# Optimization experiments

Hardware: AMD Instinct MI355X
Metric: run time of the kernel (lower is better)

Reference implementation:

```python
import math
import jax, jax.numpy as jnp
import numpy as np

HIDDEN = 768
N_HEADS = 12
HEAD_DIM = HIDDEN // N_HEADS


def _alibi_slopes(num_heads: int) -> np.ndarray:
    def pow2_slopes(n):
        start = 2.0 ** (-2.0 ** (-(math.log2(n) - 3)))
        return start ** np.arange(1, n + 1, dtype=np.float32)
    if math.log2(num_heads).is_integer():
        return pow2_slopes(num_heads).astype(np.float32)
    closest = 2 ** math.floor(math.log2(num_heads))
    base = pow2_slopes(closest)
    extra = pow2_slopes(2 * closest)[0::2][: num_heads - closest]
    return np.concatenate([base, extra], axis=0).astype(np.float32)

ALIBI_SLOPES = jnp.asarray(_alibi_slopes(N_HEADS))


def setup_inputs() -> dict:
    key = jax.random.key(0)
    ks = jax.random.split(key, 7)
    B, S = 4, 2048
    scale = 1.0 / math.sqrt(HIDDEN)
    inp = {
        "hidden_states": jax.random.normal(ks[0], (B, S, HIDDEN), dtype=jnp.float32),
        "Wq": jax.random.normal(ks[1], (HIDDEN, HIDDEN), dtype=jnp.float32) * scale,
        "bq": jnp.zeros((HIDDEN,), dtype=jnp.float32),
        "Wk": jax.random.normal(ks[2], (HIDDEN, HIDDEN), dtype=jnp.float32) * scale,
        "bk": jnp.zeros((HIDDEN,), dtype=jnp.float32),
        "Wv": jax.random.normal(ks[3], (HIDDEN, HIDDEN), dtype=jnp.float32) * scale,
        "bv": jnp.zeros((HIDDEN,), dtype=jnp.float32),
        "attention_mask": jnp.ones((B, S), dtype=jnp.int32),
    }
    return inp


def reference(hidden_states, Wq, bq, Wk, bk, Wv, bv, attention_mask):
    B, S, _ = hidden_states.shape
    H, D = N_HEADS, HEAD_DIM
    scaling = D ** (-0.5)

    # nn.Linear: x @ W.T + b, then split heads -> [B, S, H, D]
    q = (hidden_states @ Wq.T + bq).reshape(B, S, H, D)
    k = (hidden_states @ Wk.T + bk).reshape(B, S, H, D)
    v = (hidden_states @ Vv_fix(Wv, bv, hidden_states)) if False else (hidden_states @ Wv.T + bv).reshape(B, S, H, D)

    # scaled scores [B, H, Sq, Sk]
    scores = jnp.einsum("bqhd,bkhd->bhqk", q, k) * scaling

    # ALiBi bias: -slope[h] * |kv_idx - q_idx|
    pos = jnp.arange(S)
    dist = jnp.abs(pos[None, :] - pos[:, None]).astype(scores.dtype)  # [Sq, Sk]
    alibi = -ALIBI_SLOPES.astype(scores.dtype)[:, None, None] * dist  # [H, Sq, Sk]

    # padding mask over kv positions (additive min like score_mod)
    mask_penalty = jnp.finfo(scores.dtype).min
    mask_bias = jnp.where(attention_mask.astype(bool), 0.0, mask_penalty)  # [B, Sk]

    scores = scores + alibi[None] + mask_bias[:, None, None, :]
    probs = jax.nn.softmax(scores, axis=-1)

    out = jnp.einsum("bhqk,bkhd->bqhd", probs, v)  # [B, Sq, H, D]
    return out.reshape(B, S, H * D)  # dropout is no-op in eval


def Vv_fix(*a):  # unused helper kept trivially (never called)
    raise NotImplementedError
```

## Files before the change

### kernel.cpp

```cpp
#include <hip/hip_runtime.h>
#include <hip/hip_bf16.h>

#define HIDDEN 768
#define NH 12
#define HD 64
#define BB 4
#define SS 2048
#define M_TOT (BB * SS)
#define NQKV (3 * HIDDEN)
#define LOG2E 1.44269504f

typedef __attribute__((ext_vector_type(8))) short bf16x8;
typedef __attribute__((ext_vector_type(4))) float f32x4;
typedef __attribute__((ext_vector_type(4))) unsigned int u32x4;

__device__ inline unsigned short f2bf(float x) {
    __hip_bfloat16 h = __float2bfloat16(x);
    return *reinterpret_cast<unsigned short*>(&h);
}

__device__ inline void gl_lds16(const unsigned short* g, unsigned short* s) {
    __builtin_amdgcn_global_load_lds(
        (const __attribute__((address_space(1))) unsigned int*)g,
        (__attribute__((address_space(3))) unsigned int*)s, 16, 0, 0);
}

__global__ __launch_bounds__(256) void cast_kernel(
    const float* __restrict__ hs, const float* __restrict__ wq,
    const float* __restrict__ wk, const float* __restrict__ wv,
    const int* __restrict__ mask, unsigned short* __restrict__ a_bf,
    unsigned short* __restrict__ w_bf, float* __restrict__ mb,
    int* __restrict__ anym) {
    const int HS_N = M_TOT * HIDDEN / 4;
    const int W_N = HIDDEN * HIDDEN / 4;
    int idx = blockIdx.x * blockDim.x + threadIdx.x;
    if (idx < BB * SS) mb[idx] = mask[idx] ? 0.f : -1e30f;
    if (idx < BB * 32) {
        int b = idx >> 5, t = idx & 31;
        const int* mp = mask + b * SS + t * 64;
        int any = 0;
#pragma unroll 8
        for (int j = 0; j < 64; j++) any |= (mp[j] == 0);
        anym[idx] = any;
    }
    if (idx >= HS_N + 3 * W_N) return;
    if (idx < HS_N) {
        float4 v = ((const float4*)hs)[idx];
        ushort4 o;
        o.x = f2bf(v.x); o.y = f2bf(v.y); o.z = f2bf(v.z); o.w = f2bf(v.w);
        ((ushort4*)a_bf)[idx] = o;
    } else {
        int widx = idx - HS_N;
        const float* src;
        int off;
        if (widx < W_N)        { src = wq; off = widx; }
        else if (widx < 2*W_N) { src = wk; off = widx - W_N; }
        else                   { src = wv; off = widx - 2 * W_N; }
        float4 v = ((const float4*)src)[off];
        ushort4 o;
        o.x = f2bf(v.x); o.y = f2bf(v.y); o.z = f2bf(v.z); o.w = f2bf(v.w);
        ((ushort4*)w_bf)[widx] = o;
    }
}

__global__ __launch_bounds__(256, 3) void qkv_gemm(
    const unsigned short* __restrict__ A, const unsigned short* __restrict__ W,
    const float* __restrict__ bq, const float* __restrict__ bk,
    const float* __restrict__ bv, unsigned short* __restrict__ qbuf,
    unsigned short* __restrict__ kf, unsigned short* __restrict__ vf) {
    __shared__ unsigned short As[2][128][32];
    __shared__ unsigned short Bs[2][128][32];
    const int tid = threadIdx.x;
    const int m0 = blockIdx.y * 128;
    const int n0 = blockIdx.x * 128;
    const int w = tid >> 6, l = tid & 63;
    const int wm = w >> 1, wn = w & 1;
    const int lrow = l & 15;
    const int g4 = l >> 4;
    const int fcol = (g4 ^ (lrow >> 2)) * 8;

    const int srow = l >> 2;
    const int sslot = (l & 3) ^ ((l >> 4) & 3);
    const unsigned short* pA =
        A + (size_t)(m0 + w * 32 + srow) * HIDDEN + sslot * 8;
    const unsigned short* pB =
        W + (size_t)(n0 + w * 32 + srow) * HIDDEN + sslot * 8;

    f32x4 acc[4][4] = {};

#define STAGE(bb)                                          \
    do {                                                   \
        gl_lds16(pA,               &As[bb][w * 32][0]);    \
        gl_lds16(pA + 16 * HIDDEN, &As[bb][w * 32 + 16][0]); \
        gl_lds16(pB,               &Bs[bb][w * 32][0]);    \
        gl_lds16(pB + 16 * HIDDEN, &Bs[bb][w * 32 + 16][0]); \
        pA += 32; pB += 32;                                \
    } while (0)

    STAGE(0);
    __syncthreads();
    int cur = 0;

    for (int kt = 0; kt < HIDDEN / 32; kt++) {
        if (kt < HIDDEN / 32 - 1) STAGE(cur ^ 1);
        bf16x8 af[4], bfr[4];
#pragma unroll
        for (int mi = 0; mi < 4; mi++)
            af[mi] = *(const bf16x8*)&As[cur][wm * 64 + mi * 16 + lrow][fcol];
#pragma unroll
        for (int ni = 0; ni < 4; ni++)
            bfr[ni] = *(const bf16x8*)&Bs[cur][wn * 64 + ni * 16 + lrow][fcol];
        __builtin_amdgcn_s_setprio(1);
#pragma unroll
        for (int mi = 0; mi < 4; mi++)
#pragma unroll
            for (int ni = 0; ni < 4; ni++)
                acc[mi][ni] = __builtin_amdgcn_mfma_f32_16x16x32_bf16(
                    af[mi], bfr[ni], acc[mi][ni], 0, 0, 0);
        __builtin_amdgcn_s_setprio(0);
        __syncthreads();
        cur ^= 1;
    }
#undef STAGE

    if (n0 < 768) {
#pragma unroll
        for (int mi = 0; mi < 4; mi++)
#pragma unroll
            for (int ni = 0; ni < 4; ni++) {
                int col = n0 + wn * 64 + ni * 16 + lrow;
                float bias = bq[col];
#pragma unroll
                for (int i = 0; i < 4; i++) {
                    int row = m0 + wm * 64 + mi * 16 + g4 * 4 + i;
                    qbuf[(size_t)row * 768 + col] =
                        f2bf((acc[mi][ni][i] + bias) * 0.125f);
                }
            }
    } else if (n0 < 1536) {
#pragma unroll
        for (int mi = 0; mi < 4; mi++)
#pragma unroll
            for (int ni = 0; ni < 4; ni++) {
                int dd = n0 - 768 + wn * 64 + ni * 16 + lrow;
                float bias = bk[dd];
                int hh = dd >> 6, d = dd & 63;
                int gk = d >> 3, d8 = d & 7;
#pragma unroll
                for (int i = 0; i < 4; i++) {
                    int row = m0 + wm * 64 + mi * 16 + g4 * 4 + i;
                    int bb2 = row >> 11, s = row & 2047;
                    int kv16 = s >> 4, ls = s & 15;
                    kf[((size_t)(bb2 * NH + hh) * 128 + kv16) * 1024 +
                       (gk * 16 + ls) * 8 + d8] = f2bf(acc[mi][ni][i] + bias);
                }
            }
    } else {
#pragma unroll
        for (int mi = 0; mi < 4; mi++)
#pragma unroll
            for (int ni = 0; ni < 4; ni++) {
                int dd = n0 - 1536 + wn * 64 + ni * 16 + lrow;
                float bias = bv[dd];
                int hh = dd >> 6, d = dd & 63;
                int dm = d >> 4, lr = d & 15;
                int row0 = m0 + wm * 64 + mi * 16 + g4 * 4;
                int bb2 = row0 >> 11, s = row0 & 2047;
                int kv32 = s >> 5, gv = (s >> 3) & 3, s8 = s & 7;
                ushort4 o;
                o.x = f2bf(acc[mi][ni][0] + bias);
                o.y = f2bf(acc[mi][ni][1] + bias);
                o.z = f2bf(acc[mi][ni][2] + bias);
                o.w = f2bf(acc[mi][ni][3] + bias);
                *(ushort4*)(vf + (((size_t)(bb2 * NH + hh) * 4 + dm) * 64 + kv32) * 512 +
                            (gv * 16 + lr) * 8 + s8) = o;
            }
    }
}

__global__ __launch_bounds__(256) void attn_kernel(
    const unsigned short* __restrict__ Qb, const unsigned short* __restrict__ KF,
    const unsigned short* __restrict__ VF, const float* __restrict__ MB,
    const int* __restrict__ ANYM, float* __restrict__ out) {
    __shared__ unsigned short Kl[2][4096];
    __shared__ unsigned short Vl[2][4096];

    const int head_order[12] = {6, 7, 5, 4, 3, 11, 2, 10, 1, 9, 0, 8};
    const int Rtab[12]       = {31, 31, 19, 10, 5, 4, 3, 2, 2, 1, 1, 1};

    const int tid = threadIdx.x;
    const int w = tid >> 6, l = tid & 63;
    const int qt = blockIdx.x;
    const int hidx = blockIdx.y >> 2;
    const int b = blockIdx.y & 3;
    const int h = head_order[hidx];
    const int R = Rtab[hidx];
    const int bh = b * NH + h;
    const int lrow = l & 15;
    const int g = l >> 4;
    const int q = qt * 64 + w * 16 + lrow;
    const int l8 = l * 8;

    const float slope = (h < 8) ? exp2f(-(float)(h + 1))
                                : exp2f(-((float)(h - 8) + 0.5f));
    const float nslope2 = -slope * LOG2E;
    const float stp = 64.f * nslope2;

    const unsigned short* qp = Qb + (size_t)(b * SS + q) * 768 + h * HD + g * 8;
    const bf16x8 qf0 = *(const bf16x8*)(qp);
    const bf16x8 qf1 = *(const bf16x8*)(qp + 32);

    const unsigned short* kfb = KF + (size_t)bh * 128 * 1024;
    const unsigned short* vfb = VF + (size_t)bh * 4 * 64 * 512;
    const float* mbp = MB + b * SS + g * 4;
    const int* anyp = ANYM + b * 32;

    bf16x8 ones;
#pragma unroll
    for (int j = 0; j < 8; j++) ones[j] = (short)0x3F80;

    f32x4 accT[4] = {};
    f32x4 lacc = {};
    float m_run = -3.0e38f;
    float ta[16];
    bool need_full = true;

    const int kt_lo = max(0, qt - R);
    const int kt_hi = min(31, qt + R);

    {
        const unsigned short* gk0 = kfb + ((size_t)kt_lo * 4 + w) * 1024 + l8;
        const unsigned short* gv0 = vfb + ((size_t)w * 64 + kt_lo * 2) * 512 + l8;
        gl_lds16(gk0,       &Kl[0][w * 1024]);
        gl_lds16(gk0 + 512, &Kl[0][w * 1024 + 512]);
        gl_lds16(gv0,       &Vl[0][w * 1024]);
        gl_lds16(gv0 + 512, &Vl[0][w * 1024 + 512]);
    }
    __syncthreads();

    const unsigned short* gk = kfb + ((size_t)(kt_lo + 1) * 4 + w) * 1024 + l8;
    const unsigned short* gv = vfb + ((size_t)w * 64 + (size_t)(kt_lo + 1) * 2) * 512 + l8;
    int cur = 0;

    for (int kt = kt_lo; kt <= kt_hi; kt++) {
        if (kt < kt_hi) {
            gl_lds16(gk,       &Kl[cur ^ 1][w * 1024]);
            gl_lds16(gk + 512, &Kl[cur ^ 1][w * 1024 + 512]);
            gl_lds16(gv,       &Vl[cur ^ 1][w * 1024]);
            gl_lds16(gv + 512, &Vl[cur ^ 1][w * 1024 + 512]);
            gk += 4096;
            gv += 1024;
        }

        f32x4 s4[4];
        __builtin_amdgcn_s_setprio(1);
#pragma unroll
        for (int nf = 0; nf < 4; nf++) {
            bf16x8 k0 = *(const bf16x8*)&Kl[cur][nf * 1024 + l8];
            bf16x8 k1 = *(const bf16x8*)&Kl[cur][nf * 1024 + 512 + l8];
            f32x4 z = {};
            z = __builtin_amdgcn_mfma_f32_16x16x32_bf16(k0, qf0, z, 0, 0, 0);
            z = __builtin_amdgcn_mfma_f32_16x16x32_bf16(k1, qf1, z, 0, 0, 0);
            s4[nf] = z;
        }
        __builtin_amdgcn_s_setprio(0);

        if (need_full || kt == qt || kt == qt + 1) {
            const float fdf = (float)(kt * 64 + g * 4 - q);
#pragma unroll
            for (int nf = 0; nf < 4; nf++)
#pragma unroll
                for (int i = 0; i < 4; i++)
                    ta[nf * 4 + i] = fabsf(fdf + (float)(nf * 16 + i)) * nslope2;
        } else {
            const float d = (kt > qt) ? stp : -stp;
#pragma unroll
            for (int e = 0; e < 16; e++) ta[e] += d;
        }
        need_full = false;

        float sv[16];
#pragma unroll
        for (int nf = 0; nf < 4; nf++)
#pragma unroll
            for (int i = 0; i < 4; i++)
                sv[nf * 4 + i] = fmaf(s4[nf][i], LOG2E, ta[nf * 4 + i]);
        if (anyp[kt]) {
#pragma unroll
            for (int nf = 0; nf < 4; nf++) {
                float4 mbv = *(const float4*)(mbp + kt * 64 + nf * 16);
                sv[nf * 4 + 0] += mbv.x;
                sv[nf * 4 + 1] += mbv.y;
                sv[nf * 4 + 2] += mbv.z;
                sv[nf * 4 + 3] += mbv.w;
            }
        }

        float t0 = fmaxf(fmaxf(sv[0], sv[1]), sv[2]);
        float t1 = fmaxf(fmaxf(sv[3], sv[4]), sv[5]);
        float t2 = fmaxf(fmaxf(sv[6], sv[7]), sv[8]);
        float t3 = fmaxf(fmaxf(sv[9], sv[10]), sv[11]);
        float t4 = fmaxf(fmaxf(sv[12], sv[13]), sv[14]);
        float mt = fmaxf(fmaxf(fmaxf(t0, t1), fmaxf(t2, t3)), fmaxf(t4, sv[15]));
        mt = fmaxf(mt, __shfl_xor(mt, 16));
        mt = fmaxf(mt, __shfl_xor(mt, 32));

        if (!__all(mt <= m_run + 8.0f)) {
            float mnew = fmaxf(m_run, mt);
            float corr = __builtin_amdgcn_exp2f(m_run - mnew);
            m_run = mnew;
#pragma unroll
            for (int i = 0; i < 4; i++) lacc[i] *= corr;
#pragma unroll
            for (int m = 0; m < 4; m++)
#pragma unroll
                for (int i = 0; i < 4; i++) accT[m][i] *= corr;
        }

        float p[16];
#pragma unroll
        for (int e = 0; e < 16; e++)
            p[e] = __builtin_amdgcn_exp2f(sv[e] - m_run);

        unsigned pk[4][2];
#pragma unroll
        for (int nf = 0; nf < 4; nf++) {
            asm("v_cvt_pk_bf16_f32 %0, %1, %2"
                : "=v"(pk[nf][0]) : "v"(p[nf * 4 + 0]), "v"(p[nf * 4 + 1]));
            asm("v_cvt_pk_bf16_f32 %0, %1, %2"
                : "=v"(pk[nf][1]) : "v"(p[nf * 4 + 2]), "v"(p[nf * 4 + 3]));
        }

        const int dstA = ((((g & 1) << 1) | (g >> 1)) << 4) | lrow;
        const int idxA = dstA << 2;
        const int idxB = idxA ^ 128;
        const bool odd = (g & 1);
        unsigned rA0 = __builtin_amdgcn_ds_permute(idxA, (int)(odd ? pk[1][0] : pk[0][0]));
        unsigned rA1 = __builtin_amdgcn_ds_permute(idxA, (int)(odd ? pk[1][1] : pk[0][1]));
        unsigned rB0 = __builtin_amdgcn_ds_permute(idxB, (int)(odd ? pk[0][0] : pk[1][0]));
        unsigned rB1 = __builtin_amdgcn_ds_permute(idxB, (int)(odd ? pk[0][1] : pk[1][1]));
        unsigned rA2 = __builtin_amdgcn_ds_permute(idxA, (int)(odd ? pk[3][0] : pk[2][0]));
        unsigned rA3 = __builtin_amdgcn_ds_permute(idxA, (int)(odd ? pk[3][1] : pk[2][1]));
        unsigned rB2 = __builtin_amdgcn_ds_permute(idxB, (int)(odd ? pk[2][0] : pk[3][0]));
        unsigned rB3 = __builtin_amdgcn_ds_permute(idxB, (int)(odd ? pk[2][1] : pk[3][1]));
        const bool hi = (g >> 1);
        u32x4 uf0, uf1;
        uf0.x = hi ? rB0 : rA0; uf0.y = hi ? rB1 : rA1;
        uf0.z = hi ? rA0 : rB0; uf0.w = hi ? rA1 : rB1;
        uf1.x = hi ? rB2 : rA2; uf1.y = hi ? rB3 : rA3;
        uf1.z = hi ? rA2 : rB2; uf1.w = hi ? rA3 : rB3;
        bf16x8 pf0 = __builtin_bit_cast(bf16x8, uf0);
        bf16x8 pf1 = __builtin_bit_cast(bf16x8, uf1);

        __builtin_amdgcn_s_setprio(1);
#pragma unroll
        for (int m = 0; m < 4; m++) {
            bf16x8 v0 = *(const bf16x8*)&Vl[cur][m * 1024 + l8];
            bf16x8 v1 = *(const bf16x8*)&Vl[cur][m * 1024 + 512 + l8];
            accT[m] = __builtin_amdgcn_mfma_f32_16x16x32_bf16(v0, pf0, accT[m], 0, 0, 0);
            accT[m] = __builtin_amdgcn_mfma_f32_16x16x32_bf16(v1, pf1, accT[m], 0, 0, 0);
        }
        lacc = __builtin_amdgcn_mfma_f32_16x16x32_bf16(ones, pf0, lacc, 0, 0, 0);
        lacc = __builtin_amdgcn_mfma_f32_16x16x32_bf16(ones, pf1, lacc, 0, 0, 0);
        __builtin_amdgcn_s_setprio(0);

        __syncthreads();
        cur ^= 1;
    }

    const float inv = 1.0f / lacc[0];
    float* op = out + (size_t)(b * SS + q) * HIDDEN + h * HD + g * 4;
#pragma unroll
    for (int m = 0; m < 4; m++) {
        float4 o;
        o.x = accT[m][0] * inv; o.y = accT[m][1] * inv;
        o.z = accT[m][2] * inv; o.w = accT[m][3] * inv;
        *(float4*)(op + m * 16) = o;
    }
}

extern "C" void kernel_launch(void* const* d_in, const int* in_sizes, int n_in,
                              void* d_out, int out_size, void* d_ws,
                              size_t ws_size, hipStream_t stream) {
    const float* hs = (const float*)d_in[0];
    const float* wq = (const float*)d_in[1];
    const float* bq = (const float*)d_in[2];
    const float* wk = (const float*)d_in[3];
    const float* bk = (const float*)d_in[4];
    const float* wv = (const float*)d_in[5];
    const float* bv = (const float*)d_in[6];
    const int* mask = (const int*)d_in[7];
    float* out = (float*)d_out;

    unsigned short* a_bf = (unsigned short*)d_ws;
    unsigned short* w_bf = a_bf + (size_t)M_TOT * HIDDEN;
    unsigned short* qbuf = w_bf + (size_t)NQKV * HIDDEN;
    unsigned short* kf = qbuf + (size_t)M_TOT * 768;
    unsigned short* vf = kf + (size_t)BB * NH * 128 * 1024;
    float* mb = (float*)(vf + (size_t)BB * NH * 4 * 64 * 512);
    int* anym = (int*)(mb + BB * SS);

    int castN = (M_TOT * HIDDEN + 3 * HIDDEN * HIDDEN) / 4;
    cast_kernel<<<(castN + 255) / 256, 256, 0, stream>>>(
        hs, wq, wk, wv, mask, a_bf, w_bf, mb, anym);

    dim3 ggrid(NQKV / 128, M_TOT / 128);
    qkv_gemm<<<ggrid, 256, 0, stream>>>(a_bf, w_bf, bq, bk, bv, qbuf, kf, vf);

    dim3 agrid(SS / 64, BB * NH);
    attn_kernel<<<agrid, 256, 0, stream>>>(qbuf, kf, vf, mb, anym, out);
}
```

Measured before the change: 113.5 us.

## Split long-window attention heads across KV segments and merge with a combine kernel

```diff
diff --git a/kernel.cpp b/kernel.cpp
--- a/kernel.cpp
+++ b/kernel.cpp
@@ -178,6 +178,144 @@
     }
 }
 
+#define ATTN_BODY(kt_lo, kt_hi)                                               \
+    f32x4 accT[4] = {};                                                       \
+    f32x4 lacc = {};                                                          \
+    float m_run = -3.0e38f;                                                   \
+    float ta[16];                                                             \
+    bool need_full = true;                                                    \
+    {                                                                         \
+        const unsigned short* gk0 = kfb + ((size_t)(kt_lo)*4 + w) * 1024 + l8;\
+        const unsigned short* gv0 =                                           \
+            vfb + ((size_t)w * 64 + (size_t)(kt_lo)*2) * 512 + l8;            \
+        gl_lds16(gk0,       &Kl[0][w * 1024]);                                \
+        gl_lds16(gk0 + 512, &Kl[0][w * 1024 + 512]);                          \
+        gl_lds16(gv0,       &Vl[0][w * 1024]);                                \
+        gl_lds16(gv0 + 512, &Vl[0][w * 1024 + 512]);                          \
+    }                                                                         \
+    __syncthreads();                                                          \
+    const unsigned short* gk = kfb + ((size_t)((kt_lo) + 1) * 4 + w) * 1024 + l8; \
+    const unsigned short* gv =                                                \
+        vfb + ((size_t)w * 64 + (size_t)((kt_lo) + 1) * 2) * 512 + l8;        \
+    int cur = 0;                                                              \
+    for (int kt = (kt_lo); kt <= (kt_hi); kt++) {                             \
+        if (kt < (kt_hi)) {                                                   \
+            gl_lds16(gk,       &Kl[cur ^ 1][w * 1024]);                       \
+            gl_lds16(gk + 512, &Kl[cur ^ 1][w * 1024 + 512]);                 \
+            gl_lds16(gv,       &Vl[cur ^ 1][w * 1024]);                       \
+            gl_lds16(gv + 512, &Vl[cur ^ 1][w * 1024 + 512]);                 \
+            gk += 4096;                                                       \
+            gv += 1024;                                                       \
+        }                                                                     \
+        f32x4 s4[4];                                                          \
+        __builtin_amdgcn_s_setprio(1);                                        \
+        _Pragma("unroll")                                                     \
+        for (int nf = 0; nf < 4; nf++) {                                      \
+            bf16x8 k0 = *(const bf16x8*)&Kl[cur][nf * 1024 + l8];             \
+            bf16x8 k1 = *(const bf16x8*)&Kl[cur][nf * 1024 + 512 + l8];       \
+            f32x4 z = {};                                                     \
+            z = __builtin_amdgcn_mfma_f32_16x16x32_bf16(k0, qf0, z, 0, 0, 0); \
+            z = __builtin_amdgcn_mfma_f32_16x16x32_bf16(k1, qf1, z, 0, 0, 0); \
+            s4[nf] = z;                                                       \
+        }                                                                     \
+        __builtin_amdgcn_s_setprio(0);                                        \
+        if (need_full || kt == qt || kt == qt + 1) {                          \
+            const float fdf = (float)(kt * 64 + g * 4 - q);                   \
+            _Pragma("unroll")                                                 \
+            for (int nf = 0; nf < 4; nf++)                                    \
+                _Pragma("unroll")                                             \
+                for (int i = 0; i < 4; i++)                                   \
+                    ta[nf * 4 + i] =                                          \
+                        fabsf(fdf + (float)(nf * 16 + i)) * nslope2;          \
+        } else {                                                              \
+            const float d = (kt > qt) ? stp : -stp;                           \
+            _Pragma("unroll")                                                 \
+            for (int e = 0; e < 16; e++) ta[e] += d;                          \
+        }                                                                     \
+        need_full = false;                                                    \
+        float sv[16];                                                         \
+        _Pragma("unroll")                                                     \
+        for (int nf = 0; nf < 4; nf++)                                        \
+            _Pragma("unroll")                                                 \
+            for (int i = 0; i < 4; i++)                                       \
+                sv[nf * 4 + i] = fmaf(s4[nf][i], LOG2E, ta[nf * 4 + i]);      \
+        if (anyp[kt]) {                                                       \
+            _Pragma("unroll")                                                 \
+            for (int nf = 0; nf < 4; nf++) {                                  \
+                float4 mbv = *(const float4*)(mbp + kt * 64 + nf * 16);       \
+                sv[nf * 4 + 0] += mbv.x;                                      \
+                sv[nf * 4 + 1] += mbv.y;                                      \
+                sv[nf * 4 + 2] += mbv.z;                                      \
+                sv[nf * 4 + 3] += mbv.w;                                      \
+            }                                                                 \
+        }                                                                     \
+        float t0 = fmaxf(fmaxf(sv[0], sv[1]), sv[2]);                         \
+        float t1 = fmaxf(fmaxf(sv[3], sv[4]), sv[5]);                         \
+        float t2 = fmaxf(fmaxf(sv[6], sv[7]), sv[8]);                         \
+        float t3 = fmaxf(fmaxf(sv[9], sv[10]), sv[11]);                       \
+        float t4 = fmaxf(fmaxf(sv[12], sv[13]), sv[14]);                      \
+        float mt = fmaxf(fmaxf(fmaxf(t0, t1), fmaxf(t2, t3)),                 \
+                         fmaxf(t4, sv[15]));                                  \
+        mt = fmaxf(mt, __shfl_xor(mt, 16));                                   \
+        mt = fmaxf(mt, __shfl_xor(mt, 32));                                   \
+        if (!__all(mt <= m_run + 8.0f)) {                                     \
+            float mnew = fmaxf(m_run, mt);                                    \
+            float corr = __builtin_amdgcn_exp2f(m_run - mnew);                \
+            m_run = mnew;                                                     \
+            _Pragma("unroll")                                                 \
+            for (int i = 0; i < 4; i++) lacc[i] *= corr;                      \
+            _Pragma("unroll")                                                 \
+            for (int m = 0; m < 4; m++)                                       \
+                _Pragma("unroll")                                             \
+                for (int i = 0; i < 4; i++) accT[m][i] *= corr;               \
+        }                                                                     \
+        float p[16];                                                          \
+        _Pragma("unroll")                                                     \
+        for (int e = 0; e < 16; e++)                                          \
+            p[e] = __builtin_amdgcn_exp2f(sv[e] - m_run);                     \
+        unsigned pk[4][2];                                                    \
+        _Pragma("unroll")                                                     \
+        for (int nf = 0; nf < 4; nf++) {                                      \
+            asm("v_cvt_pk_bf16_f32 %0, %1, %2"                                \
+                : "=v"(pk[nf][0]) : "v"(p[nf * 4 + 0]), "v"(p[nf * 4 + 1]));  \
+            asm("v_cvt_pk_bf16_f32 %0, %1, %2"                                \
+                : "=v"(pk[nf][1]) : "v"(p[nf * 4 + 2]), "v"(p[nf * 4 + 3]));  \
+        }                                                                     \
+        const int dstA = ((((g & 1) << 1) | (g >> 1)) << 4) | lrow;           \
+        const int idxA = dstA << 2;                                           \
+        const int idxB = idxA ^ 128;                                          \
+        const bool odd = (g & 1);                                             \
+        unsigned rA0 = __builtin_amdgcn_ds_permute(idxA, (int)(odd ? pk[1][0] : pk[0][0])); \
+        unsigned rA1 = __builtin_amdgcn_ds_permute(idxA, (int)(odd ? pk[1][1] : pk[0][1])); \
+        unsigned rB0 = __builtin_amdgcn_ds_permute(idxB, (int)(odd ? pk[0][0] : pk[1][0])); \
+        unsigned rB1 = __builtin_amdgcn_ds_permute(idxB, (int)(odd ? pk[0][1] : pk[1][1])); \
+        unsigned rA2 = __builtin_amdgcn_ds_permute(idxA, (int)(odd ? pk[3][0] : pk[2][0])); \
+        unsigned rA3 = __builtin_amdgcn_ds_permute(idxA, (int)(odd ? pk[3][1] : pk[2][1])); \
+        unsigned rB2 = __builtin_amdgcn_ds_permute(idxB, (int)(odd ? pk[2][0] : pk[3][0])); \
+        unsigned rB3 = __builtin_amdgcn_ds_permute(idxB, (int)(odd ? pk[2][1] : pk[3][1])); \
+        const bool hi = (g >> 1);                                             \
+        u32x4 uf0, uf1;                                                       \
+        uf0.x = hi ? rB0 : rA0; uf0.y = hi ? rB1 : rA1;                       \
+        uf0.z = hi ? rA0 : rB0; uf0.w = hi ? rA1 : rB1;                       \
+        uf1.x = hi ? rB2 : rA2; uf1.y = hi ? rB3 : rA3;                       \
+        uf1.z = hi ? rA2 : rB2; uf1.w = hi ? rA3 : rB3;                       \
+        bf16x8 pf0 = __builtin_bit_cast(bf16x8, uf0);                         \
+        bf16x8 pf1 = __builtin_bit_cast(bf16x8, uf1);                         \
+        __builtin_amdgcn_s_setprio(1);                                        \
+        _Pragma("unroll")                                                     \
+        for (int m = 0; m < 4; m++) {                                         \
+            bf16x8 v0 = *(const bf16x8*)&Vl[cur][m * 1024 + l8];              \
+            bf16x8 v1 = *(const bf16x8*)&Vl[cur][m * 1024 + 512 + l8];        \
+            accT[m] = __builtin_amdgcn_mfma_f32_16x16x32_bf16(v0, pf0, accT[m], 0, 0, 0); \
+            accT[m] = __builtin_amdgcn_mfma_f32_16x16x32_bf16(v1, pf1, accT[m], 0, 0, 0); \
+        }                                                                     \
+        lacc = __builtin_amdgcn_mfma_f32_16x16x32_bf16(ones, pf0, lacc, 0, 0, 0); \
+        lacc = __builtin_amdgcn_mfma_f32_16x16x32_bf16(ones, pf1, lacc, 0, 0, 0); \
+        __builtin_amdgcn_s_setprio(0);                                        \
+        __syncthreads();                                                      \
+        cur ^= 1;                                                             \
+    }
+
 __global__ __launch_bounds__(256) void attn_kernel(
     const unsigned short* __restrict__ Qb, const unsigned short* __restrict__ KF,
     const unsigned short* __restrict__ VF, const float* __restrict__ MB,
@@ -219,154 +357,10 @@
 #pragma unroll
     for (int j = 0; j < 8; j++) ones[j] = (short)0x3F80;
 
-    f32x4 accT[4] = {};
-    f32x4 lacc = {};
-    float m_run = -3.0e38f;
-    float ta[16];
-    bool need_full = true;
-
     const int kt_lo = max(0, qt - R);
     const int kt_hi = min(31, qt + R);
 
-    {
-        const unsigned short* gk0 = kfb + ((size_t)kt_lo * 4 + w) * 1024 + l8;
-        const unsigned short* gv0 = vfb + ((size_t)w * 64 + kt_lo * 2) * 512 + l8;
-        gl_lds16(gk0,       &Kl[0][w * 1024]);
-        gl_lds16(gk0 + 512, &Kl[0][w * 1024 + 512]);
-        gl_lds16(gv0,       &Vl[0][w * 1024]);
-        gl_lds16(gv0 + 512, &Vl[0][w * 1024 + 512]);
-    }
-    __syncthreads();
-
-    const unsigned short* gk = kfb + ((size_t)(kt_lo + 1) * 4 + w) * 1024 + l8;
-    const unsigned short* gv = vfb + ((size_t)w * 64 + (size_t)(kt_lo + 1) * 2) * 512 + l8;
-    int cur = 0;
-
-    for (int kt = kt_lo; kt <= kt_hi; kt++) {
-        if (kt < kt_hi) {
-            gl_lds16(gk,       &Kl[cur ^ 1][w * 1024]);
-            gl_lds16(gk + 512, &Kl[cur ^ 1][w * 1024 + 512]);
-            gl_lds16(gv,       &Vl[cur ^ 1][w * 1024]);
-            gl_lds16(gv + 512, &Vl[cur ^ 1][w * 1024 + 512]);
-            gk += 4096;
-            gv += 1024;
-        }
-
-        f32x4 s4[4];
-        __builtin_amdgcn_s_setprio(1);
-#pragma unroll
-        for (int nf = 0; nf < 4; nf++) {
-            bf16x8 k0 = *(const bf16x8*)&Kl[cur][nf * 1024 + l8];
-            bf16x8 k1 = *(const bf16x8*)&Kl[cur][nf * 1024 + 512 + l8];
-            f32x4 z = {};
-            z = __builtin_amdgcn_mfma_f32_16x16x32_bf16(k0, qf0, z, 0, 0, 0);
-            z = __builtin_amdgcn_mfma_f32_16x16x32_bf16(k1, qf1, z, 0, 0, 0);
-            s4[nf] = z;
-        }
-        __builtin_amdgcn_s_setprio(0);
-
-        if (need_full || kt == qt || kt == qt + 1) {
-            const float fdf = (float)(kt * 64 + g * 4 - q);
-#pragma unroll
-            for (int nf = 0; nf < 4; nf++)
-#pragma unroll
-                for (int i = 0; i < 4; i++)
-                    ta[nf * 4 + i] = fabsf(fdf + (float)(nf * 16 + i)) * nslope2;
-        } else {
-            const float d = (kt > qt) ? stp : -stp;
-#pragma unroll
-            for (int e = 0; e < 16; e++) ta[e] += d;
-        }
-        need_full = false;
-
-        float sv[16];
-#pragma unroll
-        for (int nf = 0; nf < 4; nf++)
-#pragma unroll
-            for (int i = 0; i < 4; i++)
-                sv[nf * 4 + i] = fmaf(s4[nf][i], LOG2E, ta[nf * 4 + i]);
-        if (anyp[kt]) {
-#pragma unroll
-            for (int nf = 0; nf < 4; nf++) {
-                float4 mbv = *(const float4*)(mbp + kt * 64 + nf * 16);
-                sv[nf * 4 + 0] += mbv.x;
-                sv[nf * 4 + 1] += mbv.y;
-                sv[nf * 4 + 2] += mbv.z;
-                sv[nf * 4 + 3] += mbv.w;
-            }
-        }
-
-        float t0 = fmaxf(fmaxf(sv[0], sv[1]), sv[2]);
-        float t1 = fmaxf(fmaxf(sv[3], sv[4]), sv[5]);
-        float t2 = fmaxf(fmaxf(sv[6], sv[7]), sv[8]);
-        float t3 = fmaxf(fmaxf(sv[9], sv[10]), sv[11]);
-        float t4 = fmaxf(fmaxf(sv[12], sv[13]), sv[14]);
-        float mt = fmaxf(fmaxf(fmaxf(t0, t1), fmaxf(t2, t3)), fmaxf(t4, sv[15]));
-        mt = fmaxf(mt, __shfl_xor(mt, 16));
-        mt = fmaxf(mt, __shfl_xor(mt, 32));
-
-        if (!__all(mt <= m_run + 8.0f)) {
-            float mnew = fmaxf(m_run, mt);
-            float corr = __builtin_amdgcn_exp2f(m_run - mnew);
-            m_run = mnew;
-#pragma unroll
-            for (int i = 0; i < 4; i++) lacc[i] *= corr;
-#pragma unroll
-            for (int m = 0; m < 4; m++)
-#pragma unroll
-                for (int i = 0; i < 4; i++) accT[m][i] *= corr;
-        }
-
-        float p[16];
-#pragma unroll
-        for (int e = 0; e < 16; e++)
-            p[e] = __builtin_amdgcn_exp2f(sv[e] - m_run);
-
-        unsigned pk[4][2];
-#pragma unroll
-        for (int nf = 0; nf < 4; nf++) {
-            asm("v_cvt_pk_bf16_f32 %0, %1, %2"
-                : "=v"(pk[nf][0]) : "v"(p[nf * 4 + 0]), "v"(p[nf * 4 + 1]));
-            asm("v_cvt_pk_bf16_f32 %0, %1, %2"
-                : "=v"(pk[nf][1]) : "v"(p[nf * 4 + 2]), "v"(p[nf * 4 + 3]));
-        }
-
-        const int dstA = ((((g & 1) << 1) | (g >> 1)) << 4) | lrow;
-        const int idxA = dstA << 2;
-        const int idxB = idxA ^ 128;
-        const bool odd = (g & 1);
-        unsigned rA0 = __builtin_amdgcn_ds_permute(idxA, (int)(odd ? pk[1][0] : pk[0][0]));
-        unsigned rA1 = __builtin_amdgcn_ds_permute(idxA, (int)(odd ? pk[1][1] : pk[0][1]));
-        unsigned rB0 = __builtin_amdgcn_ds_permute(idxB, (int)(odd ? pk[0][0] : pk[1][0]));
-        unsigned rB1 = __builtin_amdgcn_ds_permute(idxB, (int)(odd ? pk[0][1] : pk[1][1]));
-        unsigned rA2 = __builtin_amdgcn_ds_permute(idxA, (int)(odd ? pk[3][0] : pk[2][0]));
-        unsigned rA3 = __builtin_amdgcn_ds_permute(idxA, (int)(odd ? pk[3][1] : pk[2][1]));
-        unsigned rB2 = __builtin_amdgcn_ds_permute(idxB, (int)(odd ? pk[2][0] : pk[3][0]));
-        unsigned rB3 = __builtin_amdgcn_ds_permute(idxB, (int)(odd ? pk[2][1] : pk[3][1]));
-        const bool hi = (g >> 1);
-        u32x4 uf0, uf1;
-        uf0.x = hi ? rB0 : rA0; uf0.y = hi ? rB1 : rA1;
-        uf0.z = hi ? rA0 : rB0; uf0.w = hi ? rA1 : rB1;
-        uf1.x = hi ? rB2 : rA2; uf1.y = hi ? rB3 : rA3;
-        uf1.z = hi ? rA2 : rB2; uf1.w = hi ? rA3 : rB3;
-        bf16x8 pf0 = __builtin_bit_cast(bf16x8, uf0);
-        bf16x8 pf1 = __builtin_bit_cast(bf16x8, uf1);
-
-        __builtin_amdgcn_s_setprio(1);
-#pragma unroll
-        for (int m = 0; m < 4; m++) {
-            bf16x8 v0 = *(const bf16x8*)&Vl[cur][m * 1024 + l8];
-            bf16x8 v1 = *(const bf16x8*)&Vl[cur][m * 1024 + 512 + l8];
-            accT[m] = __builtin_amdgcn_mfma_f32_16x16x32_bf16(v0, pf0, accT[m], 0, 0, 0);
-            accT[m] = __builtin_amdgcn_mfma_f32_16x16x32_bf16(v1, pf1, accT[m], 0, 0, 0);
-        }
-        lacc = __builtin_amdgcn_mfma_f32_16x16x32_bf16(ones, pf0, lacc, 0, 0, 0);
-        lacc = __builtin_amdgcn_mfma_f32_16x16x32_bf16(ones, pf1, lacc, 0, 0, 0);
-        __builtin_amdgcn_s_setprio(0);
-
-        __syncthreads();
-        cur ^= 1;
-    }
+    ATTN_BODY(kt_lo, kt_hi)
 
     const float inv = 1.0f / lacc[0];
     float* op = out + (size_t)(b * SS + q) * HIDDEN + h * HD + g * 4;
@@ -377,6 +371,140 @@
         o.z = accT[m][2] * inv; o.w = accT[m][3] * inv;
         *(float4*)(op + m * 16) = o;
     }
+}
+
+__global__ __launch_bounds__(256) void attn_split(
+    const unsigned short* __restrict__ Qb, const unsigned short* __restrict__ KF,
+    const unsigned short* __restrict__ VF, const float* __restrict__ MB,
+    const int* __restrict__ ANYM, float* __restrict__ out,
+    float* __restrict__ pML, float* __restrict__ pO) {
+    __shared__ unsigned short Kl[2][4096];
+    __shared__ unsigned short Vl[2][4096];
+
+    const int head_order[12] = {6, 7, 5, 4, 3, 11, 2, 10, 1, 9, 0, 8};
+    const int Rtab[12]       = {31, 31, 19, 10, 5, 4, 3, 2, 2, 1, 1, 1};
+
+    const int tid = threadIdx.x;
+    const int w = tid >> 6, l = tid & 63;
+    const int qt = blockIdx.x;
+    const int sidx = blockIdx.y >> 2;
+    const int b = blockIdx.y & 3;
+
+    int hidx, seg, S;
+    if (sidx < 8)       { hidx = sidx >> 2; seg = sidx & 3; S = 4; }
+    else if (sidx < 11) { hidx = 2;         seg = sidx - 8; S = 3; }
+    else if (sidx < 13) { hidx = 3;         seg = sidx - 11; S = 2; }
+    else                { hidx = sidx - 9;  seg = 0;         S = 1; }
+
+    const int h = head_order[hidx];
+    const int R = Rtab[hidx];
+    const int bh = b * NH + h;
+    const int lrow = l & 15;
+    const int g = l >> 4;
+    const int q = qt * 64 + w * 16 + lrow;
+    const int l8 = l * 8;
+
+    const float slope = (h < 8) ? exp2f(-(float)(h + 1))
+                                : exp2f(-((float)(h - 8) + 0.5f));
+    const float nslope2 = -slope * LOG2E;
+    const float stp = 64.f * nslope2;
+
+    const unsigned short* qp = Qb + (size_t)(b * SS + q) * 768 + h * HD + g * 8;
+    const bf16x8 qf0 = *(const bf16x8*)(qp);
+    const bf16x8 qf1 = *(const bf16x8*)(qp + 32);
+
+    const unsigned short* kfb = KF + (size_t)bh * 128 * 1024;
+    const unsigned short* vfb = VF + (size_t)bh * 4 * 64 * 512;
+    const float* mbp = MB + b * SS + g * 4;
+    const int* anyp = ANYM + b * 32;
+
+    bf16x8 ones;
+#pragma unroll
+    for (int j = 0; j < 8; j++) ones[j] = (short)0x3F80;
+
+    const int lo0 = max(0, qt - R);
+    const int hi0 = min(31, qt + R);
+    const int n = hi0 - lo0 + 1;
+    const int len = (n + S - 1) / S;
+    const int kt_lo = lo0 + seg * len;
+    const int kt_hi = min(hi0, kt_lo + len - 1);
+
+    ATTN_BODY(kt_lo, kt_hi)
+
+    if (S == 1) {
+        const float inv = 1.0f / lacc[0];
+        float* op = out + (size_t)(b * SS + q) * HIDDEN + h * HD + g * 4;
+#pragma unroll
+        for (int m = 0; m < 4; m++) {
+            float4 o;
+            o.x = accT[m][0] * inv; o.y = accT[m][1] * inv;
+            o.z = accT[m][2] * inv; o.w = accT[m][3] * inv;
+            *(float4*)(op + m * 16) = o;
+        }
+    } else {
+        float* pp = pO + ((size_t)(b * 13 + sidx) * SS + q) * 64 + g * 4;
+#pragma unroll
+        for (int m = 0; m < 4; m++) {
+            float4 o;
+            o.x = accT[m][0]; o.y = accT[m][1];
+            o.z = accT[m][2]; o.w = accT[m][3];
+            *(float4*)(pp + m * 16) = o;
+        }
+        if (g == 0) {
+            float2 ml2;
+            ml2.x = m_run;
+            ml2.y = lacc[0];
+            *(float2*)(pML + ((size_t)(b * 13 + sidx) * SS + q) * 2) = ml2;
+        }
+    }
+}
+
+__global__ __launch_bounds__(256) void combine_kernel(
+    const float* __restrict__ pML, const float* __restrict__ pO,
+    float* __restrict__ out) {
+    int t = blockIdx.x * 256 + threadIdx.x;
+    int d0 = (t & 7) * 8;
+    int row = t >> 3;
+    int q = row & 2047;
+    int hi2 = (row >> 11) & 3;
+    int b = row >> 13;
+    int S = (hi2 < 2) ? 4 : (hi2 == 2) ? 3 : 2;
+    int base = hi2 * 4 - (hi2 == 3 ? 1 : 0);
+    int h = (hi2 == 0) ? 6 : (hi2 == 1) ? 7 : (hi2 == 2) ? 5 : 4;
+
+    float m[4], lv[4];
+    float M = -3.0e38f;
+    for (int s = 0; s < S; s++) {
+        float2 ml2 = *(const float2*)(pML + ((size_t)(b * 13 + base + s) * SS + q) * 2);
+        m[s] = ml2.x;
+        lv[s] = ml2.y;
+        M = fmaxf(M, m[s]);
+    }
+    float L = 0.f;
+    float wgt[4];
+    for (int s = 0; s < S; s++) {
+        wgt[s] = exp2f(m[s] - M);
+        L += wgt[s] * lv[s];
+    }
+    const float invL = 1.0f / L;
+    float acc[8] = {};
+    for (int s = 0; s < S; s++) {
+        const float* pr = pO + ((size_t)(b * 13 + base + s) * SS + q) * 64 + d0;
+        float4 a = *(const float4*)(pr);
+        float4 c = *(const float4*)(pr + 4);
+        acc[0] += wgt[s] * a.x; acc[1] += wgt[s] * a.y;
+        acc[2] += wgt[s] * a.z; acc[3] += wgt[s] * a.w;
+        acc[4] += wgt[s] * c.x; acc[5] += wgt[s] * c.y;
+        acc[6] += wgt[s] * c.z; acc[7] += wgt[s] * c.w;
+    }
+    float* op = out + (size_t)(b * SS + q) * HIDDEN + h * HD + d0;
+    float4 o0, o1;
+    o0.x = acc[0] * invL; o0.y = acc[1] * invL;
+    o0.z = acc[2] * invL; o0.w = acc[3] * invL;
+    o1.x = acc[4] * invL; o1.y = acc[5] * invL;
+    o1.z = acc[6] * invL; o1.w = acc[7] * invL;
+    *(float4*)(op) = o0;
+    *(float4*)(op + 4) = o1;
 }
 
 extern "C" void kernel_launch(void* const* d_in, const int* in_sizes, int n_in,
@@ -399,6 +527,10 @@
     unsigned short* vf = kf + (size_t)BB * NH * 128 * 1024;
     float* mb = (float*)(vf + (size_t)BB * NH * 4 * 64 * 512);
     int* anym = (int*)(mb + BB * SS);
+    float* pml = (float*)(anym + BB * 32);
+    float* po = pml + (size_t)BB * 13 * SS * 2;
+    size_t need = (size_t)((char*)(po + (size_t)BB * 13 * SS * 64) - (char*)d_ws);
+    const bool use_split = ws_size >= need;
 
     int castN = (M_TOT * HIDDEN + 3 * HIDDEN * HIDDEN) / 4;
     cast_kernel<<<(castN + 255) / 256, 256, 0, stream>>>(
@@ -407,6 +539,12 @@
     dim3 ggrid(NQKV / 128, M_TOT / 128);
     qkv_gemm<<<ggrid, 256, 0, stream>>>(a_bf, w_bf, bq, bk, bv, qbuf, kf, vf);
 
-    dim3 agrid(SS / 64, BB * NH);
-    attn_kernel<<<agrid, 256, 0, stream>>>(qbuf, kf, vf, mb, anym, out);
-}
+    if (use_split) {
+        dim3 agrid(SS / 64, 21 * BB);
+        attn_split<<<agrid, 256, 0, stream>>>(qbuf, kf, vf, mb, anym, out, pml, po);
+        combine_kernel<<<1024, 256, 0, stream>>>(pml, po, out);
+    } else {
+        dim3 agrid(SS / 64, NH * BB);
+        attn_kernel<<<agrid, 256, 0, stream>>>(qbuf, kf, vf, mb, anym, out);
+    }
+}
```

Result: slower. 122.8 us (+8.1%).
